# Kernel optimization log

Hardware: AMD Instinct MI355X
Metric: run time of the kernel (lower is better)

Reference implementation:

```python
import jax, jax.numpy as jnp
import numpy as np

N_NODES = 100000
N_EDGES = 3200000
N_GRAPHS = 4096
IN_DIM = 74
HID = 64
MLP_HID = 128


def setup_inputs() -> dict:
    key = jax.random.key(0)
    ks = jax.random.split(key, 24)
    inp = {
        'feats': jax.random.normal(ks[0], (N_NODES, IN_DIM), jnp.float32),
        'src': jax.random.randint(ks[1], (N_EDGES,), 0, N_NODES, jnp.int32),
        'dst': jax.random.randint(ks[2], (N_EDGES,), 0, N_NODES, jnp.int32),
        'graph_ids': jnp.sort(jax.random.randint(ks[3], (N_NODES,), 0, N_GRAPHS, jnp.int32)),
    }
    dims = [IN_DIM, HID, HID, HID]
    k = 4
    for l in range(3):
        fin, fout = dims[l], dims[l + 1]
        s = 1.0 / np.sqrt(fin)
        inp[f'W{l}'] = jax.random.uniform(ks[k], (fin, fout), jnp.float32, -s, s); k += 1
        inp[f'b{l}'] = jnp.zeros((fout,), jnp.float32)
        inp[f'R{l}'] = jax.random.uniform(ks[k], (fin, fout), jnp.float32, -s, s); k += 1
        inp[f'rb{l}'] = jnp.zeros((fout,), jnp.float32)
    s = 1.0 / np.sqrt(HID)
    inp['Wm1'] = jax.random.uniform(ks[k], (HID, MLP_HID), jnp.float32, -s, s); k += 1
    inp['bm1'] = jnp.zeros((MLP_HID,), jnp.float32)
    s = 1.0 / np.sqrt(MLP_HID)
    inp['Wm2'] = jax.random.uniform(ks[k], (MLP_HID, 1), jnp.float32, -s, s)
    inp['bm2'] = jnp.zeros((1,), jnp.float32)
    return inp


def _gcn_layer(x, src, dst, W, b, R, rb):
    # GraphConv(norm='none'): h_i = sum_{j->i} x_j W + b, then ReLU
    xw = x @ W  # [N, out] -- project first (mult-first order; math identical)
    agg = jax.ops.segment_sum(xw[src], dst, num_segments=N_NODES)
    h = jax.nn.relu(agg + b)
    # dgllife residual connection: h + ReLU(Linear(x))
    return h + jax.nn.relu(x @ R + rb)


def reference(feats, src, dst, graph_ids,
              W0, b0, R0, rb0, W1, b1, R1, rb1, W2, b2, R2, rb2,
              Wm1, bm1, Wm2, bm2):
    x = _gcn_layer(feats, src, dst, W0, b0, R0, rb0)
    x = _gcn_layer(x, src, dst, W1, b1, R1, rb1)
    x = _gcn_layer(x, src, dst, W2, b2, R2, rb2)
    g = jax.ops.segment_sum(x, graph_ids, num_segments=N_GRAPHS)  # SumPooling
    h = jax.nn.relu(g @ Wm1 + bm1)
    return h @ Wm2 + bm2  # [G, 1]
```

## Files before the change

### kernel.cpp

```cpp
#include <hip/hip_runtime.h>

#define N_NODES 100000
#define N_EDGES 3200000
#define N_GRAPHS 4096
#define IN_DIM 74
#define HID 64
#define MLP_HID 128

#define BKT_NODES 128
#define NBUCKET ((N_NODES + BKT_NODES - 1) / BKT_NODES)
#define BUCKET_CAP 8192
#define NBLK 256
#define SPLIT_THREADS 1024
#define CHUNK ((N_EDGES + NBLK - 1) / NBLK)

#define STRIDE0 104
#define STRIDE12 72
#define SZ0 (64 * STRIDE0)
#define SZ12 (64 * STRIDE12)

typedef __attribute__((ext_vector_type(8))) short bf16x8;
typedef __attribute__((ext_vector_type(4))) float f32x4;

__device__ __forceinline__ unsigned short f32_to_bf16_rne(float f) {
    unsigned u = __float_as_uint(f);
    unsigned r = (u + 0x7FFFu + ((u >> 16) & 1u)) >> 16;
    return (unsigned short)r;
}
__device__ __forceinline__ float bf16u_f(unsigned short u) {
    return __uint_as_float((unsigned)u << 16);
}

#define ACC8(v, s) do { \
    a0 = fmaf((float)((int)((v).x << 24) >> 24), (s), a0); \
    a1 = fmaf((float)((int)((v).x << 16) >> 24), (s), a1); \
    a2 = fmaf((float)((int)((v).x <<  8) >> 24), (s), a2); \
    a3 = fmaf((float)((int)(v).x        >> 24), (s), a3); \
    a4 = fmaf((float)((int)((v).y << 24) >> 24), (s), a4); \
    a5 = fmaf((float)((int)((v).y << 16) >> 24), (s), a5); \
    a6 = fmaf((float)((int)((v).y <<  8) >> 24), (s), a6); \
    a7 = fmaf((float)((int)(v).y        >> 24), (s), a7); \
} while (0)

__global__ void prep_wt_kernel(const float* __restrict__ W0, const float* __restrict__ R0,
                               const float* __restrict__ W1, const float* __restrict__ R1,
                               const float* __restrict__ W2, const float* __restrict__ R2,
                               unsigned short* __restrict__ wtbuf) {
    const float* srcs[6] = {W0, R0, W1, R1, W2, R2};
    int id = blockIdx.x;
    int l = id >> 1, isR = id & 1;
    const float* src = srcs[id];
    int IN = (l == 0) ? IN_DIM : HID;
    int STRIDE = (l == 0) ? STRIDE0 : STRIDE12;
    int base = (l == 0 ? 0 : 2 * SZ0 + (l - 1) * 2 * SZ12) + isR * (l == 0 ? SZ0 : SZ12);
    int total = 64 * STRIDE;
    for (int i = threadIdx.x; i < total; i += 256) {
        int n = i / STRIDE, k = i - n * STRIDE;
        wtbuf[base + i] = (k < IN) ? f32_to_bf16_rne(src[k * HID + n]) : 0;
    }
}

template<int IN, int KPAD, int STRIDE, bool BF16IN>
__launch_bounds__(256)
__global__ void proj_mfma_kernel(const void* __restrict__ x,
                                 const unsigned short* __restrict__ wt_layer,
                                 const float* __restrict__ rb,
                                 unsigned* __restrict__ xq,
                                 float* __restrict__ xscale,
                                 unsigned short* __restrict__ resb,
                                 int n_nodes) {
    __shared__ __align__(16) unsigned short xs[64 * STRIDE];
    int n0 = blockIdx.x * 64;
    int tid = threadIdx.x;

    if (!BF16IN) {
        const float* xf = (const float*)x;
        for (int i = tid; i < 64 * STRIDE; i += 256) {
            int row = i / STRIDE, col = i - row * STRIDE;
            int n = n0 + row;
            float v = (col < IN && n < n_nodes) ? xf[(long)n * IN + col] : 0.f;
            xs[i] = f32_to_bf16_rne(v);
        }
    } else {
        const uint4* xb = (const uint4*)x;
        for (int i = tid; i < 64 * 8; i += 256) {
            int row = i >> 3, c8 = (i & 7) << 3;
            int n = n0 + row;
            uint4 v = make_uint4(0, 0, 0, 0);
            if (n < n_nodes) v = xb[(long)n * 8 + (i & 7)];
            *reinterpret_cast<uint4*>(&xs[row * STRIDE + c8]) = v;
        }
    }
    __syncthreads();

    int w = tid >> 6, lane = tid & 63;
    int nb = w * 16;
    int rc = lane & 15;
    int kg = lane >> 4;

    f32x4 accW[4], accR[4];
    #pragma unroll
    for (int fg = 0; fg < 4; ++fg) { accW[fg] = {0.f, 0.f, 0.f, 0.f}; accR[fg] = {0.f, 0.f, 0.f, 0.f}; }

    const unsigned short* wt = wt_layer;
    const unsigned short* rt = wt_layer + 64 * STRIDE;

    #pragma unroll
    for (int ks = 0; ks < KPAD / 32; ++ks) {
        int k0 = ks * 32 + kg * 8;
        bf16x8 a = *reinterpret_cast<const bf16x8*>(&xs[(nb + rc) * STRIDE + k0]);
        #pragma unroll
        for (int fg = 0; fg < 4; ++fg) {
            bf16x8 bw = *reinterpret_cast<const bf16x8*>(&wt[(fg * 16 + rc) * STRIDE + k0]);
            accW[fg] = __builtin_amdgcn_mfma_f32_16x16x32_bf16(a, bw, accW[fg], 0, 0, 0);
            bf16x8 br = *reinterpret_cast<const bf16x8*>(&rt[(fg * 16 + rc) * STRIDE + k0]);
            accR[fg] = __builtin_amdgcn_mfma_f32_16x16x32_bf16(a, br, accR[fg], 0, 0, 0);
        }
    }

    #pragma unroll
    for (int r = 0; r < 4; ++r) {
        float m = fmaxf(fmaxf(fabsf(accW[0][r]), fabsf(accW[1][r])),
                        fmaxf(fabsf(accW[2][r]), fabsf(accW[3][r])));
        m = fmaxf(m, __shfl_xor(m, 1, 64));
        m = fmaxf(m, __shfl_xor(m, 2, 64));
        m = fmaxf(m, __shfl_xor(m, 4, 64));
        m = fmaxf(m, __shfl_xor(m, 8, 64));
        float inv = (m > 0.f) ? 127.f / m : 0.f;
        int node = n0 + nb + kg * 4 + r;
        if (node < n_nodes) {
            unsigned pack = 0;
            #pragma unroll
            for (int fg = 0; fg < 4; ++fg) {
                int qv = (int)rintf(accW[fg][r] * inv);
                pack |= ((unsigned)(qv & 0xFF)) << (8 * fg);
            }
            xq[(long)node * 16 + rc] = pack;
            if (rc == 0) xscale[node] = m * (1.f / 127.f);
        }
    }
    #pragma unroll
    for (int fg = 0; fg < 4; ++fg) {
        int feat = fg * 16 + rc;
        float rbv = rb[feat];
        #pragma unroll
        for (int r = 0; r < 4; ++r) {
            int node = n0 + nb + kg * 4 + r;
            if (node < n_nodes)
                resb[(long)node * HID + feat] = f32_to_bf16_rne(fmaxf(accR[fg][r] + rbv, 0.f));
        }
    }
}

__launch_bounds__(SPLIT_THREADS)
__global__ void split_hist_kernel(const int* __restrict__ dst,
                                  int* __restrict__ blockHist ) {
    __shared__ int h[NBUCKET];
    int blk = blockIdx.x, tid = threadIdx.x;
    for (int i = tid; i < NBUCKET; i += SPLIT_THREADS) h[i] = 0;
    __syncthreads();
    int lo = blk * CHUNK;
    for (int e = lo + tid * 4; e < lo + CHUNK; e += SPLIT_THREADS * 4) {
        int4 d4 = *reinterpret_cast<const int4*>(&dst[e]);
        atomicAdd(&h[d4.x >> 7], 1);
        atomicAdd(&h[d4.y >> 7], 1);
        atomicAdd(&h[d4.z >> 7], 1);
        atomicAdd(&h[d4.w >> 7], 1);
    }
    __syncthreads();
    for (int i = tid; i < NBUCKET; i += SPLIT_THREADS)
        blockHist[i * NBLK + blk] = h[i];
}

__launch_bounds__(NBLK)
__global__ void split_scan_kernel(int* __restrict__ blockHist,
                                  int* __restrict__ cursor) {
    __shared__ int s[NBLK];
    int bkt = blockIdx.x, tid = threadIdx.x;
    int v = blockHist[bkt * NBLK + tid];
    s[tid] = v;
    __syncthreads();
    for (int off = 1; off < NBLK; off <<= 1) {
        int t = (tid >= off) ? s[tid - off] : 0;
        __syncthreads();
        s[tid] += t;
        __syncthreads();
    }
    blockHist[bkt * NBLK + tid] = bkt * BUCKET_CAP + s[tid] - v;
    if (tid == NBLK - 1) cursor[bkt] = bkt * BUCKET_CAP + s[tid];
}

__launch_bounds__(SPLIT_THREADS)
__global__ void split_scatter_kernel(const int* __restrict__ src,
                                     const int* __restrict__ dst,
                                     const int* __restrict__ blockHist,
                                     unsigned* __restrict__ pairs) {
    __shared__ int cur[NBUCKET];
    int blk = blockIdx.x, tid = threadIdx.x;
    for (int i = tid; i < NBUCKET; i += SPLIT_THREADS)
        cur[i] = blockHist[i * NBLK + blk];
    __syncthreads();
    int lo = blk * CHUNK;
    for (int e = lo + tid * 4; e < lo + CHUNK; e += SPLIT_THREADS * 4) {
        int4 d4 = *reinterpret_cast<const int4*>(&dst[e]);
        int4 s4 = *reinterpret_cast<const int4*>(&src[e]);
        int p0 = atomicAdd(&cur[d4.x >> 7], 1);
        pairs[p0] = (unsigned)s4.x | ((unsigned)(d4.x & (BKT_NODES - 1)) << 17);
        int p1 = atomicAdd(&cur[d4.y >> 7], 1);
        pairs[p1] = (unsigned)s4.y | ((unsigned)(d4.y & (BKT_NODES - 1)) << 17);
        int p2 = atomicAdd(&cur[d4.z >> 7], 1);
        pairs[p2] = (unsigned)s4.z | ((unsigned)(d4.z & (BKT_NODES - 1)) << 17);
        int p3 = atomicAdd(&cur[d4.w >> 7], 1);
        pairs[p3] = (unsigned)s4.w | ((unsigned)(d4.w & (BKT_NODES - 1)) << 17);
    }
}

__launch_bounds__(256)
__global__ void bucket_sort_kernel(unsigned* __restrict__ pairs,
                                   const int* __restrict__ cursor,
                                   int* __restrict__ row_start,
                                   int* __restrict__ row_deg) {
    __shared__ unsigned stage[BUCKET_CAP];
    __shared__ int hist[BKT_NODES];
    __shared__ int offs[BKT_NODES];
    __shared__ int cur[BKT_NODES];
    int bkt = blockIdx.x;
    int tid = threadIdx.x;
    int base = bkt * BUCKET_CAP;
    int cnt = cursor[bkt] - base;

    for (int i = tid; i < BKT_NODES; i += 256) hist[i] = 0;
    __syncthreads();
    for (int e = tid; e < cnt; e += 256) {
        unsigned p = pairs[base + e];
        stage[e] = p;
        atomicAdd(&hist[p >> 17], 1);
    }
    __syncthreads();
    if (tid < BKT_NODES) offs[tid] = hist[tid];
    __syncthreads();
    for (int s = 1; s < BKT_NODES; s <<= 1) {
        int v = (tid < BKT_NODES && tid >= s) ? offs[tid - s] : 0;
        __syncthreads();
        if (tid < BKT_NODES) offs[tid] += v;
        __syncthreads();
    }
    if (tid < BKT_NODES) {
        int ex = offs[tid] - hist[tid];
        cur[tid] = ex;
        int node = bkt * BKT_NODES + tid;
        if (node < N_NODES) {
            row_start[node] = base + ex;
            row_deg[node] = hist[tid];
        }
    }
    __syncthreads();
    for (int e = tid; e < cnt; e += 256) {
        unsigned p = stage[e];
        int pos = atomicAdd(&cur[p >> 17], 1);
        pairs[base + pos] = p & 0x1FFFF;
    }
}

__launch_bounds__(1024)
__global__ void gather_kernel(const uint2* __restrict__ xq2,
                              const float* __restrict__ xscale,
                              const int* __restrict__ row_start,
                              const int* __restrict__ row_deg,
                              const unsigned* __restrict__ csr_src,
                              const float* __restrict__ b,
                              const unsigned short* __restrict__ resb,
                              unsigned short* __restrict__ xoutb,
                              int n_nodes) {
    int wid = (blockIdx.x * blockDim.x + threadIdx.x) >> 6;
    int lane = threadIdx.x & 63;
    if (wid >= n_nodes) return;
    int g = lane >> 3;
    int c2 = lane & 7;
    int start = row_start[wid];
    int end = start + row_deg[wid];
    float a0 = 0.f, a1 = 0.f, a2 = 0.f, a3 = 0.f;
    float a4 = 0.f, a5 = 0.f, a6 = 0.f, a7 = 0.f;
    int e = start;
    unsigned sA = 0, sB = 0;
    bool have = (e + 16 <= end);
    if (have) { sA = csr_src[e + g]; sB = csr_src[e + 8 + g]; }
    while (have) {
        uint2 v0 = xq2[sA * 8 + c2]; float c0 = xscale[sA];
        uint2 v1 = xq2[sB * 8 + c2]; float c1 = xscale[sB];
        e += 16;
        have = (e + 16 <= end);
        if (have) { sA = csr_src[e + g]; sB = csr_src[e + 8 + g]; }
        ACC8(v0, c0);
        ACC8(v1, c1);
    }
    for (; e + 8 <= end; e += 8) {
        unsigned s = csr_src[e + g];
        uint2 v = xq2[s * 8 + c2]; float cs = xscale[s];
        ACC8(v, cs);
    }
    if (e < end && g < end - e) {
        unsigned s = csr_src[e + g];
        uint2 v = xq2[s * 8 + c2]; float cs = xscale[s];
        ACC8(v, cs);
    }
    a0 += __shfl_xor(a0, 8, 64); a0 += __shfl_xor(a0, 16, 64); a0 += __shfl_xor(a0, 32, 64);
    a1 += __shfl_xor(a1, 8, 64); a1 += __shfl_xor(a1, 16, 64); a1 += __shfl_xor(a1, 32, 64);
    a2 += __shfl_xor(a2, 8, 64); a2 += __shfl_xor(a2, 16, 64); a2 += __shfl_xor(a2, 32, 64);
    a3 += __shfl_xor(a3, 8, 64); a3 += __shfl_xor(a3, 16, 64); a3 += __shfl_xor(a3, 32, 64);
    a4 += __shfl_xor(a4, 8, 64); a4 += __shfl_xor(a4, 16, 64); a4 += __shfl_xor(a4, 32, 64);
    a5 += __shfl_xor(a5, 8, 64); a5 += __shfl_xor(a5, 16, 64); a5 += __shfl_xor(a5, 32, 64);
    a6 += __shfl_xor(a6, 8, 64); a6 += __shfl_xor(a6, 16, 64); a6 += __shfl_xor(a6, 32, 64);
    a7 += __shfl_xor(a7, 8, 64); a7 += __shfl_xor(a7, 16, 64); a7 += __shfl_xor(a7, 32, 64);
    if (g == 0) {
        long o = (long)wid * HID;
        int f = 2 * c2;
        #pragma unroll
        for (int blk4 = 0; blk4 < 4; ++blk4) {
            int ff = f + blk4 * 16;
            float lo_a = (blk4 == 0) ? a0 : (blk4 == 1) ? a1 : (blk4 == 2) ? a2 : a3;
            float hi_a = (blk4 == 0) ? a4 : (blk4 == 1) ? a5 : (blk4 == 2) ? a6 : a7;
            float2 bv = *reinterpret_cast<const float2*>(&b[ff]);
            unsigned rv = *reinterpret_cast<const unsigned*>(&resb[o + ff]);
            float w0 = fmaxf(lo_a + bv.x, 0.f) + __uint_as_float(rv << 16);
            float w1 = fmaxf(hi_a + bv.y, 0.f) + __uint_as_float(rv & 0xFFFF0000u);
            unsigned ov = (unsigned)f32_to_bf16_rne(w0) | ((unsigned)f32_to_bf16_rne(w1) << 16);
            *reinterpret_cast<unsigned*>(&xoutb[o + ff]) = ov;
        }
    }
}

__global__ void pool_gather_kernel(const unsigned short* __restrict__ x,
                                   const int* __restrict__ gid,
                                   float* __restrict__ g,
                                   int n_graphs) {
    int wid = (blockIdx.x * blockDim.x + threadIdx.x) >> 6;
    int lane = threadIdx.x & 63;
    if (wid >= n_graphs) return;
    int lo = 0, hi = N_NODES;
    while (lo < hi) { int mid = (lo + hi) >> 1; if (gid[mid] < wid) lo = mid + 1; else hi = mid; }
    int start = lo;
    hi = N_NODES;
    while (lo < hi) { int mid = (lo + hi) >> 1; if (gid[mid] < wid + 1) lo = mid + 1; else hi = mid; }
    int end = lo;
    float acc = 0.f;
    for (int n = start; n < end; ++n)
        acc += bf16u_f(x[(long)n * HID + lane]);
    g[(long)wid * HID + lane] = acc;
}

__global__ void mlp_kernel(const float* __restrict__ g,
                           const float* __restrict__ Wm1,
                           const float* __restrict__ bm1,
                           const float* __restrict__ Wm2,
                           const float* __restrict__ bm2,
                           float* __restrict__ out,
                           int n_graphs) {
    int wid = (blockIdx.x * blockDim.x + threadIdx.x) >> 6;
    int lane = threadIdx.x & 63;
    if (wid >= n_graphs) return;
    const float* gr = g + (long)wid * HID;
    float h0 = bm1[lane];
    float h1 = bm1[lane + 64];
    for (int k = 0; k < HID; ++k) {
        float gv = gr[k];
        h0 += gv * Wm1[k * MLP_HID + lane];
        h1 += gv * Wm1[k * MLP_HID + lane + 64];
    }
    float part = fmaxf(h0, 0.f) * Wm2[lane] + fmaxf(h1, 0.f) * Wm2[lane + 64];
    #pragma unroll
    for (int off = 32; off > 0; off >>= 1)
        part += __shfl_down(part, off, 64);
    if (lane == 0) out[wid] = part + bm2[0];
}

extern "C" void kernel_launch(void* const* d_in, const int* in_sizes, int n_in,
                              void* d_out, int out_size, void* d_ws, size_t ws_size,
                              hipStream_t stream) {
    const float* feats = (const float*)d_in[0];
    const int*   src   = (const int*)d_in[1];
    const int*   dst   = (const int*)d_in[2];
    const int*   gid   = (const int*)d_in[3];
    const float* W[3]  = {(const float*)d_in[4],  (const float*)d_in[8],  (const float*)d_in[12]};
    const float* b[3]  = {(const float*)d_in[5],  (const float*)d_in[9],  (const float*)d_in[13]};
    const float* R[3]  = {(const float*)d_in[6],  (const float*)d_in[10], (const float*)d_in[14]};
    const float* rb[3] = {(const float*)d_in[7],  (const float*)d_in[11], (const float*)d_in[15]};
    const float* Wm1 = (const float*)d_in[16];
    const float* bm1 = (const float*)d_in[17];
    const float* Wm2 = (const float*)d_in[18];
    const float* bm2 = (const float*)d_in[19];
    float* out = (float*)d_out;

    char* ws = (char*)d_ws;
    const size_t node_bf16 = (size_t)N_NODES * HID * sizeof(unsigned short);
    unsigned short* xbufb     = (unsigned short*)(ws); ws += node_bf16;
    unsigned*       xq        = (unsigned*)(ws);       ws += (size_t)N_NODES * 16 * sizeof(unsigned);
    float*          xscale    = (float*)(ws);          ws += (size_t)N_NODES * sizeof(float);
    unsigned short* resb      = (unsigned short*)(ws); ws += node_bf16;
    float*          gbuf      = (float*)(ws);          ws += (size_t)N_GRAPHS * HID * sizeof(float);
    int*            cursor    = (int*)(ws);            ws += (size_t)NBUCKET * sizeof(int);
    int*            row_start = (int*)(ws);            ws += (size_t)N_NODES * sizeof(int);
    int*            row_deg   = (int*)(ws);            ws += (size_t)N_NODES * sizeof(int);
    int*            blockHist = (int*)(ws);            ws += (size_t)NBUCKET * NBLK * sizeof(int);
    unsigned short* wtbuf     = (unsigned short*)(ws); ws += (size_t)(2 * SZ0 + 4 * SZ12) * sizeof(unsigned short);
    ws = (char*)(((size_t)ws + 255) & ~(size_t)255);
    unsigned*       pairs     = (unsigned*)(ws);       ws += (size_t)NBUCKET * BUCKET_CAP * sizeof(unsigned);

    prep_wt_kernel<<<6, 256, 0, stream>>>(W[0], R[0], W[1], R[1], W[2], R[2], wtbuf);
    split_hist_kernel<<<NBLK, SPLIT_THREADS, 0, stream>>>(dst, blockHist);
    split_scan_kernel<<<NBUCKET, NBLK, 0, stream>>>(blockHist, cursor);
    split_scatter_kernel<<<NBLK, SPLIT_THREADS, 0, stream>>>(src, dst, blockHist, pairs);
    bucket_sort_kernel<<<NBUCKET, 256, 0, stream>>>(pairs, cursor, row_start, row_deg);

    const unsigned short* wt_l[3] = {wtbuf, wtbuf + 2 * SZ0, wtbuf + 2 * SZ0 + 2 * SZ12};

    for (int l = 0; l < 3; ++l) {
        {
            int blocks = (N_NODES + 63) / 64;
            if (l == 0)
                proj_mfma_kernel<IN_DIM, 96, STRIDE0, false><<<blocks, 256, 0, stream>>>(
                    (const void*)feats, wt_l[l], rb[l], xq, xscale, resb, N_NODES);
            else
                proj_mfma_kernel<HID, 64, STRIDE12, true><<<blocks, 256, 0, stream>>>(
                    (const void*)xbufb, wt_l[l], rb[l], xq, xscale, resb, N_NODES);
        }
        {
            int blocks = (N_NODES * 64 + 1023) / 1024;
            gather_kernel<<<blocks, 1024, 0, stream>>>((const uint2*)xq, xscale, row_start, row_deg,
                                                       pairs, b[l], resb, xbufb, N_NODES);
        }
    }

    {
        int threads = N_GRAPHS * 64;
        pool_gather_kernel<<<(threads + 255) / 256, 256, 0, stream>>>(xbufb, gid, gbuf, N_GRAPHS);
    }
    {
        int threads = N_GRAPHS * 64;
        mlp_kernel<<<(threads + 255) / 256, 256, 0, stream>>>(gbuf, Wm1, bm1, Wm2, bm2, out, N_GRAPHS);
    }
}
```

Before: 363.2 us.

## Split quantized features into two feature halves and gather each in a separate pass

The projection kernel now writes the int8-quantized node features as two planar halves (feature columns split by rc>>3) instead of one interleaved 64-byte row. Aggregation runs as two launches, each gathering only one 32-byte half per edge with 16 edges per wave, so each pass's working set is half the size and more likely to stay cache-resident. The cost is reading the CSR indices and scales twice, an extra shuffle stage, and dropping the software-prefetched double-buffer loop. Block size also drops from 1024 to 256 threads.

```diff
diff --git a/kernel.cpp b/kernel.cpp
--- a/kernel.cpp
+++ b/kernel.cpp
@@ -118,6 +118,8 @@
         }
     }
 
+    unsigned* xqh = xq + (size_t)(rc >> 3) * N_NODES * 8;
+    int d = rc & 7;
     #pragma unroll
     for (int r = 0; r < 4; ++r) {
         float m = fmaxf(fmaxf(fabsf(accW[0][r]), fabsf(accW[1][r])),
@@ -135,7 +137,7 @@
                 int qv = (int)rintf(accW[fg][r] * inv);
                 pack |= ((unsigned)(qv & 0xFF)) << (8 * fg);
             }
-            xq[(long)node * 16 + rc] = pack;
+            xqh[(long)node * 8 + d] = pack;
             if (rc == 0) xscale[node] = m * (1.f / 127.f);
         }
     }
@@ -262,59 +264,47 @@
     }
 }
 
-__launch_bounds__(1024)
-__global__ void gather_kernel(const uint2* __restrict__ xq2,
-                              const float* __restrict__ xscale,
-                              const int* __restrict__ row_start,
-                              const int* __restrict__ row_deg,
-                              const unsigned* __restrict__ csr_src,
-                              const float* __restrict__ b,
-                              const unsigned short* __restrict__ resb,
-                              unsigned short* __restrict__ xoutb,
-                              int n_nodes) {
+__launch_bounds__(256)
+__global__ void gather_half_kernel(const uint2* __restrict__ xq2h,
+                                   const float* __restrict__ xscale,
+                                   const int* __restrict__ row_start,
+                                   const int* __restrict__ row_deg,
+                                   const unsigned* __restrict__ csr_src,
+                                   const float* __restrict__ b,
+                                   const unsigned short* __restrict__ resb,
+                                   unsigned short* __restrict__ xoutb,
+                                   int fbase, int n_nodes) {
     int wid = (blockIdx.x * blockDim.x + threadIdx.x) >> 6;
     int lane = threadIdx.x & 63;
     if (wid >= n_nodes) return;
-    int g = lane >> 3;
-    int c2 = lane & 7;
+    int g = lane >> 2;
+    int c2 = lane & 3;
     int start = row_start[wid];
     int end = start + row_deg[wid];
     float a0 = 0.f, a1 = 0.f, a2 = 0.f, a3 = 0.f;
     float a4 = 0.f, a5 = 0.f, a6 = 0.f, a7 = 0.f;
     int e = start;
-    unsigned sA = 0, sB = 0;
-    bool have = (e + 16 <= end);
-    if (have) { sA = csr_src[e + g]; sB = csr_src[e + 8 + g]; }
-    while (have) {
-        uint2 v0 = xq2[sA * 8 + c2]; float c0 = xscale[sA];
-        uint2 v1 = xq2[sB * 8 + c2]; float c1 = xscale[sB];
-        e += 16;
-        have = (e + 16 <= end);
-        if (have) { sA = csr_src[e + g]; sB = csr_src[e + 8 + g]; }
-        ACC8(v0, c0);
-        ACC8(v1, c1);
-    }
-    for (; e + 8 <= end; e += 8) {
+    for (; e + 16 <= end; e += 16) {
         unsigned s = csr_src[e + g];
-        uint2 v = xq2[s * 8 + c2]; float cs = xscale[s];
+        uint2 v = xq2h[(size_t)s * 4 + c2]; float cs = xscale[s];
         ACC8(v, cs);
     }
     if (e < end && g < end - e) {
         unsigned s = csr_src[e + g];
-        uint2 v = xq2[s * 8 + c2]; float cs = xscale[s];
+        uint2 v = xq2h[(size_t)s * 4 + c2]; float cs = xscale[s];
         ACC8(v, cs);
     }
-    a0 += __shfl_xor(a0, 8, 64); a0 += __shfl_xor(a0, 16, 64); a0 += __shfl_xor(a0, 32, 64);
-    a1 += __shfl_xor(a1, 8, 64); a1 += __shfl_xor(a1, 16, 64); a1 += __shfl_xor(a1, 32, 64);
-    a2 += __shfl_xor(a2, 8, 64); a2 += __shfl_xor(a2, 16, 64); a2 += __shfl_xor(a2, 32, 64);
-    a3 += __shfl_xor(a3, 8, 64); a3 += __shfl_xor(a3, 16, 64); a3 += __shfl_xor(a3, 32, 64);
-    a4 += __shfl_xor(a4, 8, 64); a4 += __shfl_xor(a4, 16, 64); a4 += __shfl_xor(a4, 32, 64);
-    a5 += __shfl_xor(a5, 8, 64); a5 += __shfl_xor(a5, 16, 64); a5 += __shfl_xor(a5, 32, 64);
-    a6 += __shfl_xor(a6, 8, 64); a6 += __shfl_xor(a6, 16, 64); a6 += __shfl_xor(a6, 32, 64);
-    a7 += __shfl_xor(a7, 8, 64); a7 += __shfl_xor(a7, 16, 64); a7 += __shfl_xor(a7, 32, 64);
+    a0 += __shfl_xor(a0, 4, 64); a0 += __shfl_xor(a0, 8, 64); a0 += __shfl_xor(a0, 16, 64); a0 += __shfl_xor(a0, 32, 64);
+    a1 += __shfl_xor(a1, 4, 64); a1 += __shfl_xor(a1, 8, 64); a1 += __shfl_xor(a1, 16, 64); a1 += __shfl_xor(a1, 32, 64);
+    a2 += __shfl_xor(a2, 4, 64); a2 += __shfl_xor(a2, 8, 64); a2 += __shfl_xor(a2, 16, 64); a2 += __shfl_xor(a2, 32, 64);
+    a3 += __shfl_xor(a3, 4, 64); a3 += __shfl_xor(a3, 8, 64); a3 += __shfl_xor(a3, 16, 64); a3 += __shfl_xor(a3, 32, 64);
+    a4 += __shfl_xor(a4, 4, 64); a4 += __shfl_xor(a4, 8, 64); a4 += __shfl_xor(a4, 16, 64); a4 += __shfl_xor(a4, 32, 64);
+    a5 += __shfl_xor(a5, 4, 64); a5 += __shfl_xor(a5, 8, 64); a5 += __shfl_xor(a5, 16, 64); a5 += __shfl_xor(a5, 32, 64);
+    a6 += __shfl_xor(a6, 4, 64); a6 += __shfl_xor(a6, 8, 64); a6 += __shfl_xor(a6, 16, 64); a6 += __shfl_xor(a6, 32, 64);
+    a7 += __shfl_xor(a7, 4, 64); a7 += __shfl_xor(a7, 8, 64); a7 += __shfl_xor(a7, 16, 64); a7 += __shfl_xor(a7, 32, 64);
     if (g == 0) {
         long o = (long)wid * HID;
-        int f = 2 * c2;
+        int f = fbase + 2 * c2;
         #pragma unroll
         for (int blk4 = 0; blk4 < 4; ++blk4) {
             int ff = f + blk4 * 16;
@@ -425,9 +415,13 @@
                     (const void*)xbufb, wt_l[l], rb[l], xq, xscale, resb, N_NODES);
         }
         {
-            int blocks = (N_NODES * 64 + 1023) / 1024;
-            gather_kernel<<<blocks, 1024, 0, stream>>>((const uint2*)xq, xscale, row_start, row_deg,
-                                                       pairs, b[l], resb, xbufb, N_NODES);
+            int blocks = (N_NODES * 64 + 255) / 256;
+            gather_half_kernel<<<blocks, 256, 0, stream>>>(
+                (const uint2*)xq, xscale, row_start, row_deg,
+                pairs, b[l], resb, xbufb, 0, N_NODES);
+            gather_half_kernel<<<blocks, 256, 0, stream>>>(
+                (const uint2*)(xq + (size_t)N_NODES * 8), xscale, row_start, row_deg,
+                pairs, b[l], resb, xbufb, 8, N_NODES);
         }
     }
 
```

Result: slower. 474.3 us (+30.6%).
